# Optimization experiments

Hardware: AMD Instinct MI355X
Metric: run time of the kernel (lower is better)

The kernel has to match this reference:

```python
import jax, jax.numpy as jnp
import numpy as np

B, T, H, S, A, E = 256, 64, 2048, 512, 64, 2048


def setup_inputs() -> dict:
    key = jax.random.key(0)
    ks = jax.random.split(key, 16)
    def w(k, shape, fan_in):
        return (jax.random.normal(k, shape, dtype=jnp.float32) / np.float32(np.sqrt(fan_in)))
    return {
        "prev_hidden": jax.random.normal(ks[0], (B, H), dtype=jnp.float32),
        "prev_state": jax.random.normal(ks[1], (B, S), dtype=jnp.float32),
        "actions": jax.random.normal(ks[2], (B, T, A), dtype=jnp.float32),
        "obs": jax.random.normal(ks[3], (B, T, E), dtype=jnp.float32),
        "prior_noise": jax.random.normal(ks[4], (B, T - 1, S), dtype=jnp.float32),
        "post_noise": jax.random.normal(ks[5], (B, T - 1, S), dtype=jnp.float32),
        # project_state_action: Linear(A+S -> H), stored [in, out]
        "W_sa": w(ks[6], (S + A, H), S + A), "b_sa": jnp.zeros((H,), jnp.float32),
        # GRUCell weights in torch layout [3H, in]
        "W_ih": w(ks[7], (3 * H, H), H), "W_hh": w(ks[8], (3 * H, H), H),
        "b_ih": jnp.zeros((3 * H,), jnp.float32), "b_hh": jnp.zeros((3 * H,), jnp.float32),
        # project_hidden_action: Linear(H+A -> H)
        "W_ha": w(ks[9], (H + A, H), H + A), "b_ha": jnp.zeros((H,), jnp.float32),
        # prior: Linear(H -> 2S)
        "W_prior": w(ks[10], (H, 2 * S), H), "b_prior": jnp.zeros((2 * S,), jnp.float32),
        # project_hidden_obs: Linear(H+E -> H)
        "W_ho": w(ks[11], (H + E, H), H + E), "b_ho": jnp.zeros((H,), jnp.float32),
        # posterior: Linear(H -> 2S)
        "W_post": w(ks[12], (H, 2 * S), H), "b_post": jnp.zeros((2 * S,), jnp.float32),
        "stop": 0,
    }


def reference(prev_hidden, prev_state, actions, obs, prior_noise, post_noise,
              W_sa, b_sa, W_ih, W_hh, b_ih, b_hh, W_ha, b_ha,
              W_prior, b_prior, W_ho, b_ho, W_post, b_post, stop):
    relu = jax.nn.relu

    def gru(x, h):
        gi = x @ W_ih.T + b_ih  # [B, 3H]
        gh = h @ W_hh.T + b_hh
        ir, iz, inn = jnp.split(gi, 3, axis=-1)
        hr, hz, hn = jnp.split(gh, 3, axis=-1)
        r = jax.nn.sigmoid(ir + hr)
        z = jax.nn.sigmoid(iz + hz)
        n = jnp.tanh(inn + r * hn)
        return (1.0 - z) * n + z * h

    def step(carry, xs):
        h, s = carry  # h: [B,H] hidden, s: [B,S] posterior state (obs is given)
        a, o, pn, qn = xs
        sa = relu(jnp.concatenate([s, a], axis=-1) @ W_sa + b_sa)
        h = gru(sa, h)
        ha = relu(jnp.concatenate([h, a], axis=-1) @ W_ha + b_ha)
        pm, plv = jnp.split(ha @ W_prior + b_prior, 2, axis=-1)
        ps = pm + jnp.exp(jax.nn.softplus(plv)) * pn  # prior rsample
        ho = relu(jnp.concatenate([h, o], axis=-1) @ W_ho + b_ho)
        qm, qlv = jnp.split(ho @ W_post + b_post, 2, axis=-1)
        qs = qm + jnp.exp(jax.nn.softplus(qlv)) * qn  # posterior rsample
        return (h, qs), (h, ps, qs, pm, plv, qm, qlv)

    Tm1 = actions.shape[1] - 1
    xs = (jnp.swapaxes(actions[:, :Tm1], 0, 1),
          jnp.swapaxes(obs[:, :Tm1], 0, 1),
          jnp.swapaxes(prior_noise, 0, 1),
          jnp.swapaxes(post_noise, 0, 1))
    _, ys = jax.lax.scan(step, (prev_hidden, prev_state), xs)
    hs, ps, qs, pm, plv, qm, qlv = (jnp.swapaxes(y, 0, 1) for y in ys)
    hiddens = jnp.concatenate([prev_hidden[:, None, :], hs], axis=1)       # [B, T, H]
    prior_states = jnp.concatenate([prev_state[:, None, :], ps], axis=1)   # [B, T, S]
    posterior_states = jnp.concatenate([prev_state[:, None, :], qs], axis=1)
    return (hiddens, prior_states, posterior_states, pm, plv, qm, qlv)
```

## Files before the change

### kernel.cpp

```cpp
#include <hip/hip_runtime.h>


typedef __attribute__((ext_vector_type(8))) short bf16x8;
typedef __attribute__((ext_vector_type(4))) float f32x4;
typedef __attribute__((ext_vector_type(4))) short s16x4;

#define DEVI static __device__ __forceinline__

DEVI float bf2f(short s) { union { float f; unsigned u; } v; v.u = ((unsigned)(unsigned short)s) << 16; return v.f; }
DEVI short f2bf(float f) {
  union { float f; unsigned u; } v; v.f = f;
  unsigned r = v.u + 0x7FFFu + ((v.u >> 16) & 1u);
  return (short)(r >> 16);
}

#define Bsz 256
#define Tsz 64
#define Hsz 2048
#define Ssz 512
#define Asz 64
#define Esz 2048
#define TM1 63

#define PSH (256 * 2048)
#define PSS (256 * 1024)

#define OUT_PS  33554432L
#define OUT_QS  41943040L
#define OUT_PM  50331648L
#define OUT_PLV 58589184L
#define OUT_QM  66846720L
#define OUT_QLV 75104256L

struct GArg {
  const short* A; const short* Bt; const float* bias; const short* Ci;
  float* oF; short* oB;
  int lda, ldb, ldoF, ldoB; long ldci, pstride;
};

template<int HASBIAS, int HASCI, int RELU, int OUTF, int OUTB>
__global__ __launch_bounds__(256) void gemm_bt(GArg g0, GArg g1, int kcK) {
  const int gemm = blockIdx.z & 1, kc = blockIdx.z >> 1;
  const GArg g = gemm ? g1 : g0;
  const short* __restrict__ Ag = g.A + (long)kc * kcK;
  const short* __restrict__ Bg = g.Bt + (long)kc * kcK;
  __shared__ __align__(16) short As[2][128 * 64];
  __shared__ __align__(16) short Bs[2][128 * 64];
  const int tid = threadIdx.x;
  const int w = tid >> 6, l = tid & 63;
  const int bm0 = blockIdx.y << 7, bn0 = blockIdx.x << 7;
  const int fc = l & 15, fh = l >> 4;
  const int wr = (w >> 1) << 6, wc = (w & 1) << 6;
  const int rx = fc & 7;

  const int srccol = ((l & 7) ^ ((l >> 3) & 7)) << 3;
  long aoff[4], boff[4];
#pragma unroll
  for (int i = 0; i < 4; ++i) {
    const int row = (((i << 2) + w) << 3) + (l >> 3);
    aoff[i] = (long)(bm0 + row) * g.lda + srccol;
    boff[i] = (long)(bn0 + row) * g.ldb + srccol;
  }

  f32x4 acc[4][4];
#pragma unroll
  for (int i = 0; i < 4; ++i)
#pragma unroll
    for (int j = 0; j < 4; ++j) acc[i][j] = f32x4{0.f, 0.f, 0.f, 0.f};

  auto STAGE = [&](int kt, int buf) {
#pragma unroll
    for (int i = 0; i < 4; ++i) {
      const int ib = ((i << 2) + w) << 10;
      __builtin_amdgcn_global_load_lds(
          (const __attribute__((address_space(1))) void*)(Ag + aoff[i] + (kt << 6)),
          (__attribute__((address_space(3))) void*)((char*)&As[buf][0] + ib), 16, 0, 0);
      __builtin_amdgcn_global_load_lds(
          (const __attribute__((address_space(1))) void*)(Bg + boff[i] + (kt << 6)),
          (__attribute__((address_space(3))) void*)((char*)&Bs[buf][0] + ib), 16, 0, 0);
    }
  };
  auto COMPUTE = [&](int buf) {
#pragma unroll
    for (int kk = 0; kk < 2; ++kk) {
      bf16x8 af[4], bb[4];
#pragma unroll
      for (int mi = 0; mi < 4; ++mi)
        af[mi] = *(const bf16x8*)&As[buf][(wr + (mi << 4) + fc) * 64 + ((((kk << 2) + fh) ^ rx) << 3)];
#pragma unroll
      for (int ni = 0; ni < 4; ++ni)
        bb[ni] = *(const bf16x8*)&Bs[buf][(wc + (ni << 4) + fc) * 64 + ((((kk << 2) + fh) ^ rx) << 3)];
#pragma unroll
      for (int mi = 0; mi < 4; ++mi)
#pragma unroll
        for (int ni = 0; ni < 4; ++ni)
          acc[mi][ni] = __builtin_amdgcn_mfma_f32_16x16x32_bf16(af[mi], bb[ni], acc[mi][ni], 0, 0, 0);
    }
  };

  const int nk = kcK >> 6;
  STAGE(0, 0);
  for (int kt = 0; kt < nk - 1; ++kt) {
    STAGE(kt + 1, (kt + 1) & 1);
    asm volatile("s_waitcnt vmcnt(8)" ::: "memory");
    __builtin_amdgcn_s_barrier();
    __builtin_amdgcn_sched_barrier(0);
    COMPUTE(kt & 1);
    asm volatile("s_waitcnt lgkmcnt(0)" ::: "memory");
    __builtin_amdgcn_s_barrier();
  }
  asm volatile("s_waitcnt vmcnt(0)" ::: "memory");
  __builtin_amdgcn_s_barrier();
  __builtin_amdgcn_sched_barrier(0);
  COMPUTE((nk - 1) & 1);

  float* oF = OUTF ? (g.oF + (long)kc * g.pstride) : (float*)nullptr;
#pragma unroll
  for (int mi = 0; mi < 4; ++mi) {
#pragma unroll
    for (int ni = 0; ni < 4; ++ni) {
      const int n = bn0 + wc + (ni << 4) + fc;
      float bv = 0.f;
      if (HASBIAS) bv = g.bias[n];
#pragma unroll
      for (int r = 0; r < 4; ++r) {
        const int m = bm0 + wr + (mi << 4) + (fh << 2) + r;
        float v = acc[mi][ni][r] + bv;
        if (HASCI) v += bf2f(g.Ci[(long)m * g.ldci + n]);
        if (RELU) v = fmaxf(v, 0.f);
        if (OUTF) oF[(long)m * g.ldoF + n] = v;
        if (OUTB) g.oB[(long)m * g.ldoB + n] = f2bf(v);
      }
    }
  }
}

__global__ void conv_f2b(const float* __restrict__ src, short* __restrict__ dst, long n) {
  long i = ((long)blockIdx.x * 256 + threadIdx.x) * 4;
  const long stride = (long)gridDim.x * 1024;
  for (; i < n; i += stride) {
    float4 v = *(const float4*)(src + i);
    s16x4 o;
    o[0] = f2bf(v.x); o[1] = f2bf(v.y); o[2] = f2bf(v.z); o[3] = f2bf(v.w);
    *(s16x4*)(dst + i) = o;
  }
}

__global__ void transp(const float* __restrict__ src, short* __restrict__ dst,
                       int srcld, int k0, int K, int N) {
  __shared__ float t[32][33];
  const int tx = threadIdx.x, ty = threadIdx.y;
  const int kb = blockIdx.y << 5, nb = blockIdx.x << 5;
#pragma unroll
  for (int i = ty; i < 32; i += 8)
    t[i][tx] = src[(long)(k0 + kb + i) * srcld + nb + tx];
  __syncthreads();
#pragma unroll
  for (int i = ty; i < 32; i += 8)
    dst[(long)(nb + i) * K + kb + tx] = f2bf(t[tx][i]);
}

__global__ void init_kernel(const float* __restrict__ ph, const float* __restrict__ ps,
                            float* __restrict__ out, short* __restrict__ hb, short* __restrict__ sb) {
  const int idx = blockIdx.x * 256 + threadIdx.x;
  const int b = idx >> 11, n = idx & 2047;
  const float h = ph[idx];
  out[(long)b * (Tsz * Hsz) + n] = h;
  hb[idx] = f2bf(h);
  if (n < Ssz) {
    const int sidx = b * Ssz + n;
    const float s = ps[sidx];
    out[OUT_PS + (long)b * (Tsz * Ssz) + n] = s;
    out[OUT_QS + (long)b * (Tsz * Ssz) + n] = s;
    sb[sidx] = f2bf(s);
  }
}

__global__ void gru_kernel(const float* __restrict__ gi, const float* __restrict__ gh,
                           const float* __restrict__ b_ih, const float* __restrict__ b_hh,
                           const float* __restrict__ hold, float* __restrict__ hnew,
                           short* __restrict__ hb) {
  const int idx = blockIdx.x * 256 + threadIdx.x;
  const int b = idx >> 11, n = idx & 2047;
  const long gb = (long)b * (3 * Hsz) + n;
  const float ir = gi[gb] + b_ih[n],                 hr = gh[gb] + b_hh[n];
  const float iz = gi[gb + Hsz] + b_ih[Hsz + n],     hz = gh[gb + Hsz] + b_hh[Hsz + n];
  const float in_ = gi[gb + 2 * Hsz] + b_ih[2 * Hsz + n];
  const float hn = gh[gb + 2 * Hsz] + b_hh[2 * Hsz + n];
  const float r = 1.f / (1.f + expf(-(ir + hr)));
  const float z = 1.f / (1.f + expf(-(iz + hz)));
  const float nn = tanhf(in_ + r * hn);
  const float h = (1.f - z) * nn + z * hold[(long)b * (Tsz * Hsz) + n];
  hnew[(long)b * (Tsz * Hsz) + n] = h;
  hb[idx] = f2bf(h);
}

__global__ void reduce_relu4(const float* __restrict__ p, const short* __restrict__ ciA,
                             const short* __restrict__ ciB, short* __restrict__ oA,
                             short* __restrict__ oB, int t) {
  const int z = blockIdx.y;
  const float* pz = p + (long)z * 4 * PSH;
  const short* ci = z ? ciB : ciA;
  short* o = z ? oB : oA;
  const int i = (blockIdx.x * 256 + threadIdx.x) * 4;
  const int b = i >> 11, n = i & 2047;
  f32x4 v = *(const f32x4*)&pz[i];
  v += *(const f32x4*)&pz[PSH + i];
  v += *(const f32x4*)&pz[2 * PSH + i];
  v += *(const f32x4*)&pz[3 * PSH + i];
  const s16x4 c = *(const s16x4*)&ci[((long)b * Tsz + t) * Hsz + n];
  s16x4 ov;
#pragma unroll
  for (int k = 0; k < 4; ++k) ov[k] = f2bf(fmaxf(v[k] + bf2f(c[k]), 0.f));
  *(s16x4*)&o[i] = ov;
}

__global__ void sample_kernel(const float* __restrict__ pp,
                              const float* __restrict__ bp, const float* __restrict__ bq,
                              const float* __restrict__ pn, const float* __restrict__ qn,
                              float* __restrict__ out, short* __restrict__ sb, int t) {
  const int idx = blockIdx.x * 256 + threadIdx.x;
  const int b = idx >> 9, j = idx & 511;
  const float* pr = pp;
  const float* po = pp + 4L * PSS;
  const long r0 = (long)b * 1024 + j;
  float pm = bp[j], plv = bp[512 + j], qm = bq[j], qlv = bq[512 + j];
#pragma unroll
  for (int k = 0; k < 4; ++k) {
    pm  += pr[k * PSS + r0];  plv += pr[k * PSS + r0 + 512];
    qm  += po[k * PSS + r0];  qlv += po[k * PSS + r0 + 512];
  }
  const long noff = ((long)b * TM1 + t) * Ssz + j;
  const float psv = pm + (1.f + expf(plv)) * pn[noff];
  const float qsv = qm + (1.f + expf(qlv)) * qn[noff];
  out[OUT_PS + (long)b * (Tsz * Ssz) + (long)(t + 1) * Ssz + j] = psv;
  out[OUT_QS + (long)b * (Tsz * Ssz) + (long)(t + 1) * Ssz + j] = qsv;
  out[OUT_PM  + noff] = pm;
  out[OUT_PLV + noff] = plv;
  out[OUT_QM  + noff] = qm;
  out[OUT_QLV + noff] = qlv;
  sb[idx] = f2bf(qsv);
}

static GArg mk(const short* A, int lda, const short* Bt, int ldb, const float* bias,
               const short* Ci, long ldci, float* oF, int ldoF, long pstride,
               short* oB, int ldoB) {
  GArg g; g.A = A; g.Bt = Bt; g.bias = bias; g.Ci = Ci; g.ldci = ldci;
  g.oF = oF; g.oB = oB; g.lda = lda; g.ldb = ldb; g.ldoF = ldoF; g.ldoB = ldoB;
  g.pstride = pstride;
  return g;
}

extern "C" void kernel_launch(void* const* d_in, const int* in_sizes, int n_in,
                              void* d_out, int out_size, void* d_ws, size_t ws_size,
                              hipStream_t stream) {
  const float* prev_hidden = (const float*)d_in[0];
  const float* prev_state  = (const float*)d_in[1];
  const float* actions     = (const float*)d_in[2];
  const float* obs         = (const float*)d_in[3];
  const float* prior_noise = (const float*)d_in[4];
  const float* post_noise  = (const float*)d_in[5];
  const float* W_sa = (const float*)d_in[6];
  const float* b_sa = (const float*)d_in[7];
  const float* W_ih = (const float*)d_in[8];
  const float* W_hh = (const float*)d_in[9];
  const float* b_ih = (const float*)d_in[10];
  const float* b_hh = (const float*)d_in[11];
  const float* W_ha = (const float*)d_in[12];
  const float* b_ha = (const float*)d_in[13];
  const float* W_prior = (const float*)d_in[14];
  const float* b_prior = (const float*)d_in[15];
  const float* W_ho = (const float*)d_in[16];
  const float* b_ho = (const float*)d_in[17];
  const float* W_post = (const float*)d_in[18];
  const float* b_post = (const float*)d_in[19];
  float* out = (float*)d_out;

  char* p = (char*)d_ws;
  auto alloc = [&](size_t bytes) { char* r = p; p += (bytes + 255) & ~(size_t)255; return r; };
  short* Wih_b   = (short*)alloc(3L * Hsz * Hsz * 2);
  short* Whh_b   = (short*)alloc(3L * Hsz * Hsz * 2);
  short* Wt_sa_s = (short*)alloc((long)Hsz * Ssz * 2);
  short* Wt_sa_a = (short*)alloc((long)Hsz * Asz * 2);
  short* Wt_ha_h = (short*)alloc((long)Hsz * Hsz * 2);
  short* Wt_ha_a = (short*)alloc((long)Hsz * Asz * 2);
  short* Wt_ho_h = (short*)alloc((long)Hsz * Hsz * 2);
  short* Wt_ho_o = (short*)alloc((long)Hsz * Esz * 2);
  short* Wt_pr   = (short*)alloc(2L * Ssz * Hsz * 2);
  short* Wt_po   = (short*)alloc(2L * Ssz * Hsz * 2);
  short* obs_b   = (short*)alloc((long)Bsz * Tsz * Esz * 2);
  short* act_b   = (short*)alloc((long)Bsz * Tsz * Asz * 2);
  short* a_pre   = (short*)alloc((long)Bsz * Tsz * Hsz * 2);
  short* ha_a    = (short*)alloc((long)Bsz * Tsz * Hsz * 2);
  short* ho_o    = (short*)alloc((long)Bsz * Tsz * Hsz * 2);
  short* s_b     = (short*)alloc((long)Bsz * Ssz * 2);
  short* h_b     = (short*)alloc((long)Bsz * Hsz * 2);
  short* sa_b    = (short*)alloc((long)Bsz * Hsz * 2);
  short* ha_b    = (short*)alloc((long)Bsz * Hsz * 2);
  short* ho_b    = (short*)alloc((long)Bsz * Hsz * 2);
  char* q = (char*)obs_b;
  auto alias = [&](size_t bytes) { char* r = q; q += (bytes + 255) & ~(size_t)255; return r; };
  float* gi_f    = (float*)alias((long)Bsz * 3 * Hsz * 4);
  float* gh_f    = (float*)alias((long)Bsz * 3 * Hsz * 4);
  float* haho_p  = (float*)alias(8L * PSH * 4);
  float* prpo_p  = (float*)alias(8L * PSS * 4);
  (void)ws_size; (void)in_sizes; (void)n_in; (void)out_size;

  conv_f2b<<<4096, 256, 0, stream>>>(obs,  obs_b, (long)Bsz * Tsz * Esz);
  conv_f2b<<<1024, 256, 0, stream>>>(actions, act_b, (long)Bsz * Tsz * Asz);
  conv_f2b<<<4096, 256, 0, stream>>>(W_ih, Wih_b, 3L * Hsz * Hsz);
  conv_f2b<<<4096, 256, 0, stream>>>(W_hh, Whh_b, 3L * Hsz * Hsz);

  dim3 tb(32, 8);
  transp<<<dim3(Hsz / 32, Ssz / 32), tb, 0, stream>>>(W_sa, Wt_sa_s, Hsz, 0,   Ssz, Hsz);
  transp<<<dim3(Hsz / 32, Asz / 32), tb, 0, stream>>>(W_sa, Wt_sa_a, Hsz, Ssz, Asz, Hsz);
  transp<<<dim3(Hsz / 32, Hsz / 32), tb, 0, stream>>>(W_ha, Wt_ha_h, Hsz, 0,   Hsz, Hsz);
  transp<<<dim3(Hsz / 32, Asz / 32), tb, 0, stream>>>(W_ha, Wt_ha_a, Hsz, Hsz, Asz, Hsz);
  transp<<<dim3(Hsz / 32, Hsz / 32), tb, 0, stream>>>(W_ho, Wt_ho_h, Hsz, 0,   Hsz, Hsz);
  transp<<<dim3(Hsz / 32, Esz / 32), tb, 0, stream>>>(W_ho, Wt_ho_o, Hsz, Hsz, Esz, Hsz);
  transp<<<dim3(2 * Ssz / 32, Hsz / 32), tb, 0, stream>>>(W_prior, Wt_pr, 2 * Ssz, 0, Hsz, 2 * Ssz);
  transp<<<dim3(2 * Ssz / 32, Hsz / 32), tb, 0, stream>>>(W_post,  Wt_po, 2 * Ssz, 0, Hsz, 2 * Ssz);

  init_kernel<<<2048, 256, 0, stream>>>(prev_hidden, prev_state, out, h_b, s_b);

  {
    GArg g0 = mk(act_b, Asz, Wt_sa_a, Asz, b_sa, nullptr, 0, nullptr, 0, 0, a_pre, Hsz);
    GArg g1 = mk(act_b, Asz, Wt_ha_a, Asz, b_ha, nullptr, 0, nullptr, 0, 0, ha_a, Hsz);
    gemm_bt<1, 0, 0, 0, 1><<<dim3(Hsz / 128, (Bsz * Tsz) / 128, 2), 256, 0, stream>>>(g0, g1, Asz);
  }
  {
    GArg g0 = mk(obs_b, Esz, Wt_ho_o, Esz, b_ho, nullptr, 0, nullptr, 0, 0, ho_o, Hsz);
    gemm_bt<1, 0, 0, 0, 1><<<dim3(Hsz / 128, (Bsz * Tsz) / 128, 1), 256, 0, stream>>>(g0, g0, Esz);
  }

  const long ldPre = (long)Tsz * Hsz;
  for (int t = 0; t < TM1; ++t) {
    {
      GArg g0 = mk(s_b, Ssz, Wt_sa_s, Ssz, nullptr, a_pre + (long)t * Hsz, ldPre,
                   nullptr, 0, 0, sa_b, Hsz);
      gemm_bt<0, 1, 1, 0, 1><<<dim3(16, 2, 1), 256, 0, stream>>>(g0, g0, Ssz);
    }
    {
      GArg g0 = mk(sa_b, Hsz, Wih_b, Hsz, nullptr, nullptr, 0, gi_f, 3 * Hsz, 0, nullptr, 0);
      GArg g1 = mk(h_b,  Hsz, Whh_b, Hsz, nullptr, nullptr, 0, gh_f, 3 * Hsz, 0, nullptr, 0);
      gemm_bt<0, 0, 0, 1, 0><<<dim3(48, 2, 2), 256, 0, stream>>>(g0, g1, Hsz);
    }
    gru_kernel<<<2048, 256, 0, stream>>>(gi_f, gh_f, b_ih, b_hh,
                                         out + (long)t * Hsz, out + (long)(t + 1) * Hsz, h_b);
    {
      GArg g0 = mk(h_b, Hsz, Wt_ha_h, Hsz, nullptr, nullptr, 0, haho_p, Hsz, PSH, nullptr, 0);
      GArg g1 = mk(h_b, Hsz, Wt_ho_h, Hsz, nullptr, nullptr, 0, haho_p + 4L * PSH, Hsz, PSH, nullptr, 0);
      gemm_bt<0, 0, 0, 1, 0><<<dim3(16, 2, 8), 256, 0, stream>>>(g0, g1, Hsz / 4);
    }
    reduce_relu4<<<dim3(512, 2), 256, 0, stream>>>(haho_p, ha_a, ho_o, ha_b, ho_b, t);
    {
      GArg g0 = mk(ha_b, Hsz, Wt_pr, Hsz, nullptr, nullptr, 0, prpo_p, 2 * Ssz, PSS, nullptr, 0);
      GArg g1 = mk(ho_b, Hsz, Wt_po, Hsz, nullptr, nullptr, 0, prpo_p + 4L * PSS, 2 * Ssz, PSS, nullptr, 0);
      gemm_bt<0, 0, 0, 1, 0><<<dim3(8, 2, 8), 256, 0, stream>>>(g0, g1, Hsz / 4);
    }
    sample_kernel<<<512, 256, 0, stream>>>(prpo_p, b_prior, b_post,
                                           prior_noise, post_noise, out, s_b, t);
  }
}
```

Before: 6.638 ms.

## Use full-batch 256x64 GEMM tiles and bf16 intermediates in recurrent step

Adds a gemm_n64 kernel whose block covers all 256 batch rows and a 64-column strip, so each weight tile is loaded once per step instead of once per 128-row block. All per-step GEMMs switch to it, with twice as many column blocks. The GRU gate pre-activations and the split-K partial sums for the hidden and prior/posterior projections are now stored as bf16 instead of fp32, cutting intermediate memory traffic. The GRU kernel is vectorised to handle four elements per thread. The cost is lower precision in the partial sums and gate values, plus a larger LDS footprint per block.

```diff
diff --git a/kernel.cpp b/kernel.cpp
--- a/kernel.cpp
+++ b/kernel.cpp
@@ -22,8 +22,8 @@
 #define Esz 2048
 #define TM1 63
 
-#define PSH (256 * 2048)
-#define PSS (256 * 1024)
+#define PSHB (256 * 2048)
+#define PSSB (256 * 1024)
 
 #define OUT_PS  33554432L
 #define OUT_QS  41943040L
@@ -39,20 +39,128 @@
 };
 
 template<int HASBIAS, int HASCI, int RELU, int OUTF, int OUTB>
-__global__ __launch_bounds__(256) void gemm_bt(GArg g0, GArg g1, int kcK) {
-  const int gemm = blockIdx.z & 1, kc = blockIdx.z >> 1;
+__global__ __launch_bounds__(256) void gemm_n64(GArg g0, GArg g1, int glog, int kcK) {
+  const int z = blockIdx.z;
+  const int gemm = glog ? (z & 1) : 0;
+  const int kc = z >> glog;
   const GArg g = gemm ? g1 : g0;
   const short* __restrict__ Ag = g.A + (long)kc * kcK;
   const short* __restrict__ Bg = g.Bt + (long)kc * kcK;
-  __shared__ __align__(16) short As[2][128 * 64];
-  __shared__ __align__(16) short Bs[2][128 * 64];
+  __shared__ __align__(16) short As[2][16384];
+  __shared__ __align__(16) short Bs[2][4096];
+  const int tid = threadIdx.x;
+  const int w = tid >> 6, l = tid & 63;
+  const int bn0 = blockIdx.x << 6;
+  const int fc = l & 15, fh = l >> 4;
+  const int wr = w << 6;
+  const int rx = fc & 7;
+  const int srccol = ((l & 7) ^ ((l >> 3) & 7)) << 3;
+
+  long aoff[8], boff[2];
+#pragma unroll
+  for (int i = 0; i < 8; ++i) {
+    const int row = (((i << 2) + w) << 3) + (l >> 3);
+    aoff[i] = (long)row * g.lda + srccol;
+  }
+#pragma unroll
+  for (int i = 0; i < 2; ++i) {
+    const int row = (((i << 2) + w) << 3) + (l >> 3);
+    boff[i] = (long)(bn0 + row) * g.ldb + srccol;
+  }
+
+  f32x4 acc[4][4];
+#pragma unroll
+  for (int i = 0; i < 4; ++i)
+#pragma unroll
+    for (int j = 0; j < 4; ++j) acc[i][j] = f32x4{0.f, 0.f, 0.f, 0.f};
+
+  auto STAGE = [&](int kt, int buf) {
+#pragma unroll
+    for (int i = 0; i < 8; ++i) {
+      const int ib = ((i << 2) + w) << 10;
+      __builtin_amdgcn_global_load_lds(
+          (const __attribute__((address_space(1))) void*)(Ag + aoff[i] + (kt << 6)),
+          (__attribute__((address_space(3))) void*)((char*)&As[buf][0] + ib), 16, 0, 0);
+    }
+#pragma unroll
+    for (int i = 0; i < 2; ++i) {
+      const int ib = ((i << 2) + w) << 10;
+      __builtin_amdgcn_global_load_lds(
+          (const __attribute__((address_space(1))) void*)(Bg + boff[i] + (kt << 6)),
+          (__attribute__((address_space(3))) void*)((char*)&Bs[buf][0] + ib), 16, 0, 0);
+    }
+  };
+  auto COMPUTE = [&](int buf) {
+#pragma unroll
+    for (int kk = 0; kk < 2; ++kk) {
+      const int sw = (((kk << 2) + fh) ^ rx) << 3;
+      bf16x8 af[4], bb[4];
+#pragma unroll
+      for (int mi = 0; mi < 4; ++mi)
+        af[mi] = *(const bf16x8*)&As[buf][(wr + (mi << 4) + fc) * 64 + sw];
+#pragma unroll
+      for (int ni = 0; ni < 4; ++ni)
+        bb[ni] = *(const bf16x8*)&Bs[buf][((ni << 4) + fc) * 64 + sw];
+#pragma unroll
+      for (int mi = 0; mi < 4; ++mi)
+#pragma unroll
+        for (int ni = 0; ni < 4; ++ni)
+          acc[mi][ni] = __builtin_amdgcn_mfma_f32_16x16x32_bf16(af[mi], bb[ni], acc[mi][ni], 0, 0, 0);
+    }
+  };
+
+  const int nk = kcK >> 6;
+  STAGE(0, 0);
+  for (int kt = 0; kt < nk - 1; ++kt) {
+    STAGE(kt + 1, (kt + 1) & 1);
+    asm volatile("s_waitcnt vmcnt(10)" ::: "memory");
+    __builtin_amdgcn_s_barrier();
+    __builtin_amdgcn_sched_barrier(0);
+    COMPUTE(kt & 1);
+    asm volatile("s_waitcnt lgkmcnt(0)" ::: "memory");
+    __builtin_amdgcn_s_barrier();
+  }
+  asm volatile("s_waitcnt vmcnt(0)" ::: "memory");
+  __builtin_amdgcn_s_barrier();
+  __builtin_amdgcn_sched_barrier(0);
+  COMPUTE((nk - 1) & 1);
+
+  float* oF = OUTF ? (g.oF + (long)kc * g.pstride) : (float*)nullptr;
+  short* oB = OUTB ? (g.oB + (long)kc * g.pstride) : (short*)nullptr;
+#pragma unroll
+  for (int mi = 0; mi < 4; ++mi) {
+#pragma unroll
+    for (int ni = 0; ni < 4; ++ni) {
+      const int n = bn0 + (ni << 4) + fc;
+      float bv = 0.f;
+      if (HASBIAS) bv = g.bias[n];
+#pragma unroll
+      for (int r = 0; r < 4; ++r) {
+        const int m = wr + (mi << 4) + (fh << 2) + r;
+        float v = acc[mi][ni][r] + bv;
+        if (HASCI) v += bf2f(g.Ci[(long)m * g.ldci + n]);
+        if (RELU) v = fmaxf(v, 0.f);
+        if (OUTF) oF[(long)m * g.ldoF + n] = v;
+        if (OUTB) oB[(long)m * g.ldoB + n] = f2bf(v);
+      }
+    }
+  }
+}
+
+template<int HASBIAS, int HASCI, int RELU, int OUTF, int OUTB>
+__global__ __launch_bounds__(256) void gemm_bt(GArg g0, GArg g1, int kcK) {
+  const int gemm = blockIdx.z & 1;
+  const GArg g = gemm ? g1 : g0;
+  const short* __restrict__ Ag = g.A;
+  const short* __restrict__ Bg = g.Bt;
+  __shared__ __align__(16) short As[2][8192];
+  __shared__ __align__(16) short Bs[2][8192];
   const int tid = threadIdx.x;
   const int w = tid >> 6, l = tid & 63;
   const int bm0 = blockIdx.y << 7, bn0 = blockIdx.x << 7;
   const int fc = l & 15, fh = l >> 4;
   const int wr = (w >> 1) << 6, wc = (w & 1) << 6;
   const int rx = fc & 7;
-
   const int srccol = ((l & 7) ^ ((l >> 3) & 7)) << 3;
   long aoff[4], boff[4];
 #pragma unroll
@@ -61,7 +169,6 @@
     aoff[i] = (long)(bm0 + row) * g.lda + srccol;
     boff[i] = (long)(bn0 + row) * g.ldb + srccol;
   }
-
   f32x4 acc[4][4];
 #pragma unroll
   for (int i = 0; i < 4; ++i)
@@ -114,7 +221,6 @@
   __builtin_amdgcn_sched_barrier(0);
   COMPUTE((nk - 1) & 1);
 
-  float* oF = OUTF ? (g.oF + (long)kc * g.pstride) : (float*)nullptr;
 #pragma unroll
   for (int mi = 0; mi < 4; ++mi) {
 #pragma unroll
@@ -128,7 +234,7 @@
         float v = acc[mi][ni][r] + bv;
         if (HASCI) v += bf2f(g.Ci[(long)m * g.ldci + n]);
         if (RELU) v = fmaxf(v, 0.f);
-        if (OUTF) oF[(long)m * g.ldoF + n] = v;
+        if (OUTF) g.oF[(long)m * g.ldoF + n] = v;
         if (OUTB) g.oB[(long)m * g.ldoB + n] = f2bf(v);
       }
     }
@@ -176,59 +282,78 @@
   }
 }
 
-__global__ void gru_kernel(const float* __restrict__ gi, const float* __restrict__ gh,
+__global__ void gru_kernel(const short* __restrict__ gi, const short* __restrict__ gh,
                            const float* __restrict__ b_ih, const float* __restrict__ b_hh,
                            const float* __restrict__ hold, float* __restrict__ hnew,
                            short* __restrict__ hb) {
-  const int idx = blockIdx.x * 256 + threadIdx.x;
-  const int b = idx >> 11, n = idx & 2047;
+  const int i4 = (blockIdx.x * 256 + threadIdx.x) * 4;
+  const int b = i4 >> 11, n = i4 & 2047;
   const long gb = (long)b * (3 * Hsz) + n;
-  const float ir = gi[gb] + b_ih[n],                 hr = gh[gb] + b_hh[n];
-  const float iz = gi[gb + Hsz] + b_ih[Hsz + n],     hz = gh[gb + Hsz] + b_hh[Hsz + n];
-  const float in_ = gi[gb + 2 * Hsz] + b_ih[2 * Hsz + n];
-  const float hn = gh[gb + 2 * Hsz] + b_hh[2 * Hsz + n];
-  const float r = 1.f / (1.f + expf(-(ir + hr)));
-  const float z = 1.f / (1.f + expf(-(iz + hz)));
-  const float nn = tanhf(in_ + r * hn);
-  const float h = (1.f - z) * nn + z * hold[(long)b * (Tsz * Hsz) + n];
-  hnew[(long)b * (Tsz * Hsz) + n] = h;
-  hb[idx] = f2bf(h);
-}
-
-__global__ void reduce_relu4(const float* __restrict__ p, const short* __restrict__ ciA,
+  const s16x4 vir = *(const s16x4*)&gi[gb];
+  const s16x4 viz = *(const s16x4*)&gi[gb + Hsz];
+  const s16x4 vin = *(const s16x4*)&gi[gb + 2 * Hsz];
+  const s16x4 vhr = *(const s16x4*)&gh[gb];
+  const s16x4 vhz = *(const s16x4*)&gh[gb + Hsz];
+  const s16x4 vhn = *(const s16x4*)&gh[gb + 2 * Hsz];
+  const float4 ho = *(const float4*)&hold[(long)b * (Tsz * Hsz) + n];
+  const float* hop = (const float*)&ho;
+  float4 hv; float* hvp = (float*)&hv;
+  s16x4 hbv;
+#pragma unroll
+  for (int e = 0; e < 4; ++e) {
+    const int ne = n + e;
+    const float ir = bf2f(vir[e]) + b_ih[ne],           hr = bf2f(vhr[e]) + b_hh[ne];
+    const float iz = bf2f(viz[e]) + b_ih[Hsz + ne],     hz = bf2f(vhz[e]) + b_hh[Hsz + ne];
+    const float in_ = bf2f(vin[e]) + b_ih[2 * Hsz + ne];
+    const float hn = bf2f(vhn[e]) + b_hh[2 * Hsz + ne];
+    const float r = 1.f / (1.f + expf(-(ir + hr)));
+    const float zz = 1.f / (1.f + expf(-(iz + hz)));
+    const float nn = tanhf(in_ + r * hn);
+    const float h = (1.f - zz) * nn + zz * hop[e];
+    hvp[e] = h;
+    hbv[e] = f2bf(h);
+  }
+  *(float4*)&hnew[(long)b * (Tsz * Hsz) + n] = hv;
+  *(s16x4*)&hb[i4] = hbv;
+}
+
+__global__ void reduce_relu4(const short* __restrict__ p, const short* __restrict__ ciA,
                              const short* __restrict__ ciB, short* __restrict__ oA,
                              short* __restrict__ oB, int t) {
   const int z = blockIdx.y;
-  const float* pz = p + (long)z * 4 * PSH;
+  const short* pz = p + (long)z * 4 * PSHB;
   const short* ci = z ? ciB : ciA;
   short* o = z ? oB : oA;
   const int i = (blockIdx.x * 256 + threadIdx.x) * 4;
   const int b = i >> 11, n = i & 2047;
-  f32x4 v = *(const f32x4*)&pz[i];
-  v += *(const f32x4*)&pz[PSH + i];
-  v += *(const f32x4*)&pz[2 * PSH + i];
-  v += *(const f32x4*)&pz[3 * PSH + i];
+  float v[4] = {0.f, 0.f, 0.f, 0.f};
+#pragma unroll
+  for (int k = 0; k < 4; ++k) {
+    const s16x4 pk = *(const s16x4*)&pz[(long)k * PSHB + i];
+#pragma unroll
+    for (int e = 0; e < 4; ++e) v[e] += bf2f(pk[e]);
+  }
   const s16x4 c = *(const s16x4*)&ci[((long)b * Tsz + t) * Hsz + n];
   s16x4 ov;
 #pragma unroll
-  for (int k = 0; k < 4; ++k) ov[k] = f2bf(fmaxf(v[k] + bf2f(c[k]), 0.f));
+  for (int e = 0; e < 4; ++e) ov[e] = f2bf(fmaxf(v[e] + bf2f(c[e]), 0.f));
   *(s16x4*)&o[i] = ov;
 }
 
-__global__ void sample_kernel(const float* __restrict__ pp,
+__global__ void sample_kernel(const short* __restrict__ pp,
                               const float* __restrict__ bp, const float* __restrict__ bq,
                               const float* __restrict__ pn, const float* __restrict__ qn,
                               float* __restrict__ out, short* __restrict__ sb, int t) {
   const int idx = blockIdx.x * 256 + threadIdx.x;
   const int b = idx >> 9, j = idx & 511;
-  const float* pr = pp;
-  const float* po = pp + 4L * PSS;
+  const short* pr = pp;
+  const short* po = pp + 4L * PSSB;
   const long r0 = (long)b * 1024 + j;
   float pm = bp[j], plv = bp[512 + j], qm = bq[j], qlv = bq[512 + j];
 #pragma unroll
   for (int k = 0; k < 4; ++k) {
-    pm  += pr[k * PSS + r0];  plv += pr[k * PSS + r0 + 512];
-    qm  += po[k * PSS + r0];  qlv += po[k * PSS + r0 + 512];
+    pm  += bf2f(pr[k * PSSB + r0]);  plv += bf2f(pr[k * PSSB + r0 + 512]);
+    qm  += bf2f(po[k * PSSB + r0]);  qlv += bf2f(po[k * PSSB + r0 + 512]);
   }
   const long noff = ((long)b * TM1 + t) * Ssz + j;
   const float psv = pm + (1.f + expf(plv)) * pn[noff];
@@ -300,10 +425,10 @@
   short* ho_b    = (short*)alloc((long)Bsz * Hsz * 2);
   char* q = (char*)obs_b;
   auto alias = [&](size_t bytes) { char* r = q; q += (bytes + 255) & ~(size_t)255; return r; };
-  float* gi_f    = (float*)alias((long)Bsz * 3 * Hsz * 4);
-  float* gh_f    = (float*)alias((long)Bsz * 3 * Hsz * 4);
-  float* haho_p  = (float*)alias(8L * PSH * 4);
-  float* prpo_p  = (float*)alias(8L * PSS * 4);
+  short* gi_b    = (short*)alias((long)Bsz * 3 * Hsz * 2);
+  short* gh_b    = (short*)alias((long)Bsz * 3 * Hsz * 2);
+  short* haho_pb = (short*)alias(8L * PSHB * 2);
+  short* prpo_pb = (short*)alias(8L * PSSB * 2);
   (void)ws_size; (void)in_sizes; (void)n_in; (void)out_size;
 
   conv_f2b<<<4096, 256, 0, stream>>>(obs,  obs_b, (long)Bsz * Tsz * Esz);
@@ -338,27 +463,27 @@
     {
       GArg g0 = mk(s_b, Ssz, Wt_sa_s, Ssz, nullptr, a_pre + (long)t * Hsz, ldPre,
                    nullptr, 0, 0, sa_b, Hsz);
-      gemm_bt<0, 1, 1, 0, 1><<<dim3(16, 2, 1), 256, 0, stream>>>(g0, g0, Ssz);
+      gemm_n64<0, 1, 1, 0, 1><<<dim3(32, 1, 1), 256, 0, stream>>>(g0, g0, 0, Ssz);
     }
     {
-      GArg g0 = mk(sa_b, Hsz, Wih_b, Hsz, nullptr, nullptr, 0, gi_f, 3 * Hsz, 0, nullptr, 0);
-      GArg g1 = mk(h_b,  Hsz, Whh_b, Hsz, nullptr, nullptr, 0, gh_f, 3 * Hsz, 0, nullptr, 0);
-      gemm_bt<0, 0, 0, 1, 0><<<dim3(48, 2, 2), 256, 0, stream>>>(g0, g1, Hsz);
-    }
-    gru_kernel<<<2048, 256, 0, stream>>>(gi_f, gh_f, b_ih, b_hh,
-                                         out + (long)t * Hsz, out + (long)(t + 1) * Hsz, h_b);
+      GArg g0 = mk(sa_b, Hsz, Wih_b, Hsz, nullptr, nullptr, 0, nullptr, 0, 0, gi_b, 3 * Hsz);
+      GArg g1 = mk(h_b,  Hsz, Whh_b, Hsz, nullptr, nullptr, 0, nullptr, 0, 0, gh_b, 3 * Hsz);
+      gemm_n64<0, 0, 0, 0, 1><<<dim3(96, 1, 2), 256, 0, stream>>>(g0, g1, 1, Hsz);
+    }
+    gru_kernel<<<512, 256, 0, stream>>>(gi_b, gh_b, b_ih, b_hh,
+                                        out + (long)t * Hsz, out + (long)(t + 1) * Hsz, h_b);
     {
-      GArg g0 = mk(h_b, Hsz, Wt_ha_h, Hsz, nullptr, nullptr, 0, haho_p, Hsz, PSH, nullptr, 0);
-      GArg g1 = mk(h_b, Hsz, Wt_ho_h, Hsz, nullptr, nullptr, 0, haho_p + 4L * PSH, Hsz, PSH, nullptr, 0);
-      gemm_bt<0, 0, 0, 1, 0><<<dim3(16, 2, 8), 256, 0, stream>>>(g0, g1, Hsz / 4);
-    }
-    reduce_relu4<<<dim3(512, 2), 256, 0, stream>>>(haho_p, ha_a, ho_o, ha_b, ho_b, t);
+      GArg g0 = mk(h_b, Hsz, Wt_ha_h, Hsz, nullptr, nullptr, 0, nullptr, 0, PSHB, haho_pb, Hsz);
+      GArg g1 = mk(h_b, Hsz, Wt_ho_h, Hsz, nullptr, nullptr, 0, nullptr, 0, PSHB, haho_pb + 4L * PSHB, Hsz);
+      gemm_n64<0, 0, 0, 0, 1><<<dim3(32, 1, 8), 256, 0, stream>>>(g0, g1, 1, Hsz / 4);
+    }
+    reduce_relu4<<<dim3(512, 2), 256, 0, stream>>>(haho_pb, ha_a, ho_o, ha_b, ho_b, t);
     {
-      GArg g0 = mk(ha_b, Hsz, Wt_pr, Hsz, nullptr, nullptr, 0, prpo_p, 2 * Ssz, PSS, nullptr, 0);
-      GArg g1 = mk(ho_b, Hsz, Wt_po, Hsz, nullptr, nullptr, 0, prpo_p + 4L * PSS, 2 * Ssz, PSS, nullptr, 0);
-      gemm_bt<0, 0, 0, 1, 0><<<dim3(8, 2, 8), 256, 0, stream>>>(g0, g1, Hsz / 4);
-    }
-    sample_kernel<<<512, 256, 0, stream>>>(prpo_p, b_prior, b_post,
+      GArg g0 = mk(ha_b, Hsz, Wt_pr, Hsz, nullptr, nullptr, 0, nullptr, 0, PSSB, prpo_pb, 2 * Ssz);
+      GArg g1 = mk(ho_b, Hsz, Wt_po, Hsz, nullptr, nullptr, 0, nullptr, 0, PSSB, prpo_pb + 4L * PSSB, 2 * Ssz);
+      gemm_n64<0, 0, 0, 0, 1><<<dim3(16, 1, 8), 256, 0, stream>>>(g0, g1, 1, Hsz / 4);
+    }
+    sample_kernel<<<512, 256, 0, stream>>>(prpo_pb, b_prior, b_post,
                                            prior_noise, post_noise, out, s_b, t);
   }
 }
```

Result: slower. 6.791 ms (+2.3%).
